# Optimization experiments

Measured on AMD Instinct MI355X. Metric: run time of the kernel, lower is better.

## Reference

```python
import jax, jax.numpy as jnp
import numpy as np

NUM_HEADS = 16


def setup_inputs() -> dict:
    key = jax.random.key(0)
    ks = jax.random.split(key, 5)
    B, S, D = 2, 2048, 2048
    scale = 1.0 / np.sqrt(D)
    return {
        "x": jax.random.normal(ks[0], (B, S, D), dtype=jnp.float32),
        "W_q": jax.random.normal(ks[1], (D, D), dtype=jnp.float32) * scale,
        "W_k": jax.random.normal(ks[2], (D, D), dtype=jnp.float32) * scale,
        "W_v": jax.random.normal(ks[3], (D, D), dtype=jnp.float32) * scale,
        "W_o": jax.random.normal(ks[4], (D, D), dtype=jnp.float32) * scale,
        "b_o": jnp.zeros((D,), dtype=jnp.float32),
    }


def reference(x, W_q, W_k, W_v, W_o, b_o):
    B, S, D = x.shape
    H = NUM_HEADS
    hd = D // H
    # projections, split into heads: [B, H, S, hd]
    q = (x @ W_q).reshape(B, S, H, hd).transpose(0, 2, 1, 3)
    k = (x @ W_k).reshape(B, S, H, hd).transpose(0, 2, 1, 3)
    v = (x @ W_v).reshape(B, S, H, hd).transpose(0, 2, 1, 3)
    # causal attention with explicit score matrix [B, H, S, S]
    scores = jnp.einsum("bhqd,bhkd->bhqk", q, k) / jnp.sqrt(jnp.asarray(hd, x.dtype))
    causal = jnp.tril(jnp.ones((S, S), dtype=bool))  # True = keep
    scores = jnp.where(causal, scores, -jnp.inf)
    weights = jax.nn.softmax(scores, axis=-1)
    ctx = jnp.einsum("bhqk,bhkd->bhqd", weights, v)
    ctx = ctx.transpose(0, 2, 1, 3).reshape(B, S, D)
    return ctx @ W_o + b_o
```

## Files before the change

### kernel.cpp

```cpp
#include <hip/hip_runtime.h>
#include <stdint.h>

#define SQ_S 2048
#define DIM 2048
#define NH 16
#define HD 128
#define NB 2
#define NROWS (NB * SQ_S)
#define NQKV (3 * DIM)
#define NQK (2 * DIM)

typedef __bf16 bf16x8 __attribute__((ext_vector_type(8)));
typedef float f32x4 __attribute__((ext_vector_type(4)));
typedef unsigned short u16;

__device__ __forceinline__ u16 f2bf(float f) {
    unsigned int u = __float_as_uint(f);
    u += 0x7FFF + ((u >> 16) & 1);
    return (u16)(u >> 16);
}

__device__ __forceinline__ void load_lds16(const u16* g, u16* lds) {
    __builtin_amdgcn_global_load_lds(
        (const __attribute__((address_space(1))) unsigned int*)(uintptr_t)g,
        (__attribute__((address_space(3))) unsigned int*)(unsigned int)(uintptr_t)lds,
        16, 0, 0);
}

__global__ __launch_bounds__(256) void cast_x_kernel(const float* __restrict__ in,
                                                     u16* __restrict__ out) {
    int i = (blockIdx.x * 256 + threadIdx.x) * 4;
    float4 v = *(const float4*)(in + i);
    ushort4 o;
    o.x = f2bf(v.x); o.y = f2bf(v.y); o.z = f2bf(v.z); o.w = f2bf(v.w);
    *(ushort4*)(out + i) = o;
}

__global__ __launch_bounds__(256) void transpose_w_kernel(
    const float* __restrict__ w0, const float* __restrict__ w1,
    const float* __restrict__ w2, const float* __restrict__ w3,
    u16* __restrict__ o0, u16* __restrict__ o1,
    u16* __restrict__ o2, u16* __restrict__ o3) {
    __shared__ u16 tile[64][65];
    int z = blockIdx.z;
    const float* in = z == 0 ? w0 : z == 1 ? w1 : z == 2 ? w2 : w3;
    u16* out = z == 0 ? o0 : z == 1 ? o1 : z == 2 ? o2 : o3;
    int r0 = blockIdx.y * 64, c0 = blockIdx.x * 64;
    int t = threadIdx.x;
#pragma unroll
    for (int i = 0; i < 16; ++i) {
        int idx = i * 256 + t;
        int r = idx >> 6, c = idx & 63;
        tile[r][c] = f2bf(in[(size_t)(r0 + r) * DIM + c0 + c]);
    }
    __syncthreads();
#pragma unroll
    for (int i = 0; i < 4; ++i) {
        int idx = i * 256 + t;
        int oc = idx >> 4;
        int r4 = (idx & 15) * 4;
        ushort4 v;
        v.x = tile[r4 + 0][oc]; v.y = tile[r4 + 1][oc];
        v.z = tile[r4 + 2][oc]; v.w = tile[r4 + 3][oc];
        *(ushort4*)(out + (size_t)(c0 + oc) * DIM + r0 + r4) = v;
    }
}

#define NTK (DIM / 64)

__device__ __forceinline__ bf16x8 frag(const u16* half, int row, int lq) {
    return *(const bf16x8*)(half + row * 32 + (((lq + (row >> 1)) & 3) * 8));
}

__device__ __forceinline__ void stage_half(const u16* __restrict__ G, int grow0, int gcol0,
                                           u16* dst, int t) {
#pragma unroll
    for (int i = 0; i < 2; ++i) {
        int e = (i * 512 + t) * 8;
        int r = e >> 5;
        int c = ((t & 3) - (r >> 1)) & 3;
        load_lds16(G + (size_t)(grow0 + r) * DIM + gcol0 + c * 8, dst + e);
    }
}

#define HSZ (256 * 32)

__global__ __launch_bounds__(512) void gemm_qkv(const u16* __restrict__ A,
                                                const u16* __restrict__ Bt,
                                                u16* __restrict__ QKo,
                                                u16* __restrict__ Vt) {
    __shared__ u16 As[2][2][HSZ];
    __shared__ u16 Bs[2][2][HSZ];
    int bid = blockIdx.x;
    int wg = (bid & 7) * 48 + (bid >> 3);
    int bm = wg / 24, bn = wg % 24;
    int gm0 = bm * 256, gn0 = bn * 256;
    int t = threadIdx.x;
    int w = t >> 6, l = t & 63;
    int wm = w >> 2, wn = w & 3;
    int lr = l & 15, lq = l >> 4;
    int ar = wm * 128 + lr;
    int br = wn * 64 + lr;
    f32x4 acc[8][4] = {};
    bf16x8 af[4], bfr[4];

    stage_half(A,  gm0, 0,  As[0][0], t);
    stage_half(Bt, gn0, 0,  Bs[0][0], t);
    stage_half(A,  gm0, 32, As[0][1], t);
    stage_half(Bt, gn0, 32, Bs[0][1], t);
    asm volatile("s_waitcnt vmcnt(4)" ::: "memory");
    __builtin_amdgcn_s_barrier();

#pragma unroll 2
    for (int kt = 0; kt < NTK; ++kt) {
        int buf = kt & 1, nbuf = buf ^ 1;
        int ks = (kt + 1 < NTK) ? kt + 1 : kt;
#pragma unroll
        for (int kk = 0; kk < 2; ++kk) {
            const u16* ah = As[buf][kk];
            const u16* bh = Bs[buf][kk];
#pragma unroll
            for (int nf = 0; nf < 4; ++nf) bfr[nf] = frag(bh, br + nf * 16, lq);
#pragma unroll
            for (int mf = 0; mf < 4; ++mf) af[mf] = frag(ah, ar + mf * 16, lq);
            stage_half(A, gm0, ks * 64 + kk * 32, As[nbuf][kk], t);
            __builtin_amdgcn_s_barrier();
            __builtin_amdgcn_s_setprio(1);
#pragma unroll
            for (int mf = 0; mf < 4; ++mf)
#pragma unroll
                for (int nf = 0; nf < 4; ++nf)
                    acc[mf][nf] = __builtin_amdgcn_mfma_f32_16x16x32_bf16(af[mf], bfr[nf], acc[mf][nf], 0, 0, 0);
            __builtin_amdgcn_s_setprio(0);
            __builtin_amdgcn_s_barrier();
#pragma unroll
            for (int mf = 0; mf < 4; ++mf) af[mf] = frag(ah, ar + 64 + mf * 16, lq);
            stage_half(Bt, gn0, ks * 64 + kk * 32, Bs[nbuf][kk], t);
            asm volatile("s_waitcnt vmcnt(4)" ::: "memory");
            __builtin_amdgcn_s_barrier();
            __builtin_amdgcn_s_setprio(1);
#pragma unroll
            for (int mf = 0; mf < 4; ++mf)
#pragma unroll
                for (int nf = 0; nf < 4; ++nf)
                    acc[mf + 4][nf] = __builtin_amdgcn_mfma_f32_16x16x32_bf16(af[mf], bfr[nf], acc[mf + 4][nf], 0, 0, 0);
            __builtin_amdgcn_s_setprio(0);
            __builtin_amdgcn_s_barrier();
        }
    }
    asm volatile("s_waitcnt vmcnt(0)" ::: "memory");

    int c0g = gn0 + wn * 64;
    int r0g = gm0 + wm * 128;
    if (bn < 16) {
#pragma unroll
        for (int mf = 0; mf < 8; ++mf)
#pragma unroll
            for (int nf = 0; nf < 4; ++nf) {
                int col = c0g + nf * 16 + lr;
                int rowb = r0g + mf * 16 + lq * 4;
#pragma unroll
                for (int r = 0; r < 4; ++r)
                    QKo[(size_t)(rowb + r) * NQK + col] = f2bf(acc[mf][nf][r]);
            }
    } else {
#pragma unroll
        for (int mf = 0; mf < 8; ++mf)
#pragma unroll
            for (int nf = 0; nf < 4; ++nf) {
                int colv = c0g + nf * 16 + lr - 4096;
                int h = colv >> 7, dd = colv & 127;
                int rowb = r0g + mf * 16 + lq * 4;
                int b = rowb >> 11, s = rowb & 2047;
                ushort4 v4;
                v4.x = f2bf(acc[mf][nf][0]);
                v4.y = f2bf(acc[mf][nf][1]);
                v4.z = f2bf(acc[mf][nf][2]);
                v4.w = f2bf(acc[mf][nf][3]);
                *(ushort4*)(Vt + (((size_t)(b * NH + h) * HD + dd) * SQ_S + s)) = v4;
            }
    }
}

#define ASZ (256 * 32)
#define BSZ (128 * 32)

__device__ __forceinline__ void stage_b128(const u16* __restrict__ Bt, int gn0, int kt, int kk,
                                           u16* dst, int t) {
    int e = t * 8;
    int r = e >> 5;
    int c = ((t & 3) - (r >> 1)) & 3;
    load_lds16(Bt + (size_t)(gn0 + r) * DIM + kt * 64 + kk * 32 + c * 8, dst + e);
}

__device__ __forceinline__ void gemm_core(const u16* __restrict__ A, const u16* __restrict__ Bt,
                                          int gm0, int gn0, u16* As, u16* Bs,
                                          f32x4 acc[4][4]) {
    int t = threadIdx.x;
    int w = t >> 6, l = t & 63;
    int wm = w >> 1, wn = w & 1;
    int lr = l & 15, lq = l >> 4;
    int ar = wm * 64 + lr;
    int br = wn * 64 + lr;

    stage_half(A, gm0, 0, As + 0 * ASZ, t);
    stage_b128(Bt, gn0, 0, 0, Bs + 0 * BSZ, t);
    stage_half(A, gm0, 32, As + 1 * ASZ, t);
    stage_b128(Bt, gn0, 0, 1, Bs + 1 * BSZ, t);
    stage_half(A, gm0, 64, As + 2 * ASZ, t);
    stage_b128(Bt, gn0, 1, 0, Bs + 2 * BSZ, t);
    asm volatile("s_waitcnt vmcnt(6)" ::: "memory");
    __builtin_amdgcn_s_barrier();

#pragma unroll 2
    for (int kt = 0; kt < NTK; ++kt) {
        int buf = kt & 1, nbuf = buf ^ 1;
        const u16* a0 = As + (buf * 2 + 0) * ASZ;
        const u16* a1 = As + (buf * 2 + 1) * ASZ;
        const u16* b0 = Bs + (buf * 2 + 0) * BSZ;
        const u16* b1 = Bs + (buf * 2 + 1) * BSZ;
        bf16x8 af[4], bfr[4];

#pragma unroll
        for (int mf = 0; mf < 4; ++mf) af[mf] = frag(a0, ar + mf * 16, lq);
#pragma unroll
        for (int nf = 0; nf < 4; ++nf) bfr[nf] = frag(b0, br + nf * 16, lq);
        {
            int ks = (kt + 1 < NTK) ? kt + 1 : kt;
            stage_half(A, gm0, ks * 64 + 32, As + (nbuf * 2 + 1) * ASZ, t);
            stage_b128(Bt, gn0, ks, 1, Bs + (nbuf * 2 + 1) * BSZ, t);
        }
        asm volatile("s_waitcnt vmcnt(6)" ::: "memory");
        __builtin_amdgcn_s_barrier();
        __builtin_amdgcn_s_setprio(1);
#pragma unroll
        for (int mf = 0; mf < 4; ++mf)
#pragma unroll
            for (int nf = 0; nf < 4; ++nf)
                acc[mf][nf] = __builtin_amdgcn_mfma_f32_16x16x32_bf16(af[mf], bfr[nf], acc[mf][nf], 0, 0, 0);
        __builtin_amdgcn_s_setprio(0);
        __builtin_amdgcn_s_barrier();

#pragma unroll
        for (int mf = 0; mf < 4; ++mf) af[mf] = frag(a1, ar + mf * 16, lq);
#pragma unroll
        for (int nf = 0; nf < 4; ++nf) bfr[nf] = frag(b1, br + nf * 16, lq);
        {
            int ks = (kt + 2 < NTK) ? kt + 2 : kt;
            stage_half(A, gm0, ks * 64, As + (buf * 2 + 0) * ASZ, t);
            stage_b128(Bt, gn0, ks, 0, Bs + (buf * 2 + 0) * BSZ, t);
        }
        asm volatile("s_waitcnt vmcnt(6)" ::: "memory");
        __builtin_amdgcn_s_barrier();
        __builtin_amdgcn_s_setprio(1);
#pragma unroll
        for (int mf = 0; mf < 4; ++mf)
#pragma unroll
            for (int nf = 0; nf < 4; ++nf)
                acc[mf][nf] = __builtin_amdgcn_mfma_f32_16x16x32_bf16(af[mf], bfr[nf], acc[mf][nf], 0, 0, 0);
        __builtin_amdgcn_s_setprio(0);
        __builtin_amdgcn_s_barrier();
    }
    asm volatile("s_waitcnt vmcnt(0)" ::: "memory");
}

__global__ __launch_bounds__(512) void gemm_out(const u16* __restrict__ A,
                                                const u16* __restrict__ Bt,
                                                float* __restrict__ C,
                                                const float* __restrict__ bias) {
    __shared__ u16 As[4 * ASZ];
    __shared__ u16 Bs[4 * BSZ];
    int bid = blockIdx.x;
    int wg = (bid & 7) * 32 + (bid >> 3);
    int bm = wg >> 4, bn = wg & 15;
    f32x4 acc[4][4] = {};
    gemm_core(A, Bt, bm * 256, bn * 128, As, Bs, acc);

    int t = threadIdx.x, w = t >> 6, l = t & 63;
    int wm = w >> 1, wn = w & 1, lr = l & 15, lq = l >> 4;
    int r0 = bm * 256 + wm * 64;
    int c0 = bn * 128 + wn * 64;
#pragma unroll
    for (int mf = 0; mf < 4; ++mf)
#pragma unroll
        for (int nf = 0; nf < 4; ++nf) {
            int col = c0 + nf * 16 + lr;
            float bb = bias[col];
            int rowb = r0 + mf * 16 + lq * 4;
#pragma unroll
            for (int r = 0; r < 4; ++r)
                C[(size_t)(rowb + r) * DIM + col] = acc[mf][nf][r] + bb;
        }
}

__global__ __launch_bounds__(256) void attn_kernel(const u16* __restrict__ Q,
                                                   const u16* __restrict__ K,
                                                   const u16* __restrict__ Vt,
                                                   u16* __restrict__ ctx, int ldqk) {
    __shared__ u16 Kl[2][64 * 128];
    __shared__ u16 Vl[2][128 * 64];
    __shared__ u16 Pl[4][16 * 64];
    int t = threadIdx.x;
    int w = t >> 6, l = t & 63;
    int lr = l & 15, q = l >> 4, lk = q * 8;
    int bid = blockIdx.x;
    int r_  = bid >> 3;
    int px  = r_ & 15;
    int h   = (bid & 7) + ((r_ >> 4) & 1) * 8;
    int b   = r_ >> 5;
    const float scale = 0.08838834764831845f;
    int stK_gcol = (((t & 15) ^ (t >> 4)) * 8);
    int stV_gcol = (((t & 7) ^ ((t >> 3) & 7)) * 8);
    const u16* Kbase = K + (size_t)b * SQ_S * ldqk + h * HD;
    const u16* Vbase = Vt + ((size_t)(b * NH + h)) * HD * SQ_S;

    bf16x8 vones;
#pragma unroll
    for (int i = 0; i < 8; ++i) vones[i] = (__bf16)1.0f;

#pragma unroll 1
    for (int pass = 0; pass < 2; ++pass) {
        int qt = pass == 0 ? px : 31 - px;
        int q0 = qt * 64;
        int njt = qt + 1;

        bf16x8 qf[4];
        {
            const u16* qp = Q + ((size_t)(b * SQ_S + q0 + w * 16 + lr)) * ldqk + h * HD;
#pragma unroll
            for (int kd = 0; kd < 4; ++kd)
                qf[kd] = *(const bf16x8*)(qp + kd * 32 + lk);
        }

        f32x4 o[8] = {};
        f32x4 lsum = {0.f, 0.f, 0.f, 0.f};

        {
            int e = t * 8;
#pragma unroll
            for (int c = 0; c < 4; ++c) {
                int eK = c * 2048 + e;
                load_lds16(Kbase + (size_t)(eK >> 7) * ldqk + stK_gcol, Kl[0] + eK);
            }
#pragma unroll
            for (int c = 0; c < 4; ++c) {
                int eV = c * 2048 + e;
                load_lds16(Vbase + (size_t)(eV >> 6) * SQ_S + stV_gcol, Vl[0] + eV);
            }
        }

#pragma unroll 1
        for (int jt = 0; jt < njt; ++jt) {
            __syncthreads();
            if (jt + 1 < njt) {
                int j1 = (jt + 1) * 64;
                u16* Kd = Kl[(jt + 1) & 1];
                u16* Vd = Vl[(jt + 1) & 1];
                int e = t * 8;
#pragma unroll
                for (int c = 0; c < 4; ++c) {
                    int eK = c * 2048 + e;
                    load_lds16(Kbase + (size_t)(j1 + (eK >> 7)) * ldqk + stK_gcol, Kd + eK);
                }
#pragma unroll
                for (int c = 0; c < 4; ++c) {
                    int eV = c * 2048 + e;
                    load_lds16(Vbase + (size_t)(eV >> 6) * SQ_S + j1 + stV_gcol, Vd + eV);
                }
            }
            const u16* Kc = Kl[jt & 1];
            const u16* Vc = Vl[jt & 1];

            f32x4 s[4] = {};
            __builtin_amdgcn_s_setprio(1);
#pragma unroll
            for (int kd = 0; kd < 4; ++kd) {
#pragma unroll
                for (int nt = 0; nt < 4; ++nt) {
                    bf16x8 kb = *(const bf16x8*)(Kc + (nt * 16 + lr) * 128 +
                                                 (((kd * 4 + q) ^ lr) * 8));
                    s[nt] = __builtin_amdgcn_mfma_f32_16x16x32_bf16(qf[kd], kb, s[nt], 0, 0, 0);
                }
            }
            __builtin_amdgcn_s_setprio(0);
            bool diag = (jt == qt);
            float pv[4][4];
#pragma unroll
            for (int nt = 0; nt < 4; ++nt)
#pragma unroll
                for (int r = 0; r < 4; ++r) {
                    float v = s[nt][r] * scale - 6.0f;
                    if (diag && (nt * 16 + lr > w * 16 + q * 4 + r)) v = -1.0e30f;
                    pv[nt][r] = __expf(v);
                }
            u16* pw = Pl[w];
#pragma unroll
            for (int nt = 0; nt < 4; ++nt)
#pragma unroll
                for (int r = 0; r < 4; ++r) {
                    int prow = q * 4 + r;
                    int pcol = nt * 16 + lr;
                    pw[prow * 64 + (((pcol >> 3) ^ (prow & 7)) * 8) + (pcol & 7)] = f2bf(pv[nt][r]);
                }
            asm volatile("s_waitcnt lgkmcnt(0)" ::: "memory");
            __builtin_amdgcn_s_setprio(1);
#pragma unroll
            for (int kj = 0; kj < 2; ++kj) {
                bf16x8 pa = *(const bf16x8*)(pw + lr * 64 + (((kj * 4 + q) ^ (lr & 7)) * 8));
                lsum = __builtin_amdgcn_mfma_f32_16x16x32_bf16(pa, vones, lsum, 0, 0, 0);
#pragma unroll
                for (int nd = 0; nd < 8; ++nd) {
                    bf16x8 vb = *(const bf16x8*)(Vc + (nd * 16 + lr) * 64 +
                                                 (((kj * 4 + q) ^ (lr & 7)) * 8));
                    o[nd] = __builtin_amdgcn_mfma_f32_16x16x32_bf16(pa, vb, o[nd], 0, 0, 0);
                }
            }
            __builtin_amdgcn_s_setprio(0);
        }
        float li[4];
#pragma unroll
        for (int r = 0; r < 4; ++r) li[r] = 1.f / lsum[r];
#pragma unroll
        for (int nd = 0; nd < 8; ++nd)
#pragma unroll
            for (int r = 0; r < 4; ++r) {
                int row = q0 + w * 16 + q * 4 + r;
                int col = h * HD + nd * 16 + lr;
                ctx[((size_t)(b * SQ_S + row)) * DIM + col] = f2bf(o[nd][r] * li[r]);
            }
        __syncthreads();
    }
}

extern "C" void kernel_launch(void* const* d_in, const int* in_sizes, int n_in,
                              void* d_out, int out_size, void* d_ws, size_t ws_size,
                              hipStream_t stream) {
    const float* x  = (const float*)d_in[0];
    const float* Wq = (const float*)d_in[1];
    const float* Wk = (const float*)d_in[2];
    const float* Wv = (const float*)d_in[3];
    const float* Wo = (const float*)d_in[4];
    const float* bo = (const float*)d_in[5];
    float* out = (float*)d_out;

    char* p = (char*)d_ws;
    const size_t SZ_ACT = (size_t)NROWS * DIM * 2;
    const size_t SZ_W   = (size_t)DIM * DIM * 2;
    u16* Xb   = (u16*)(p);
    u16* Wqkv = (u16*)(p + SZ_ACT);
    u16* Wot  = (u16*)(p + SZ_ACT + 3 * SZ_W);
    u16* QK   = (u16*)(p + SZ_ACT + 4 * SZ_W);
    u16* Vt   = (u16*)(p + 3 * SZ_ACT + 4 * SZ_W);
    u16* Cx   = (u16*)(p + 4 * SZ_ACT + 4 * SZ_W);

    cast_x_kernel<<<(NROWS * DIM) / 1024, 256, 0, stream>>>(x, Xb);
    transpose_w_kernel<<<dim3(DIM / 64, DIM / 64, 4), 256, 0, stream>>>(
        Wq, Wk, Wv, Wo,
        Wqkv, Wqkv + (size_t)DIM * DIM, Wqkv + 2 * (size_t)DIM * DIM, Wot);
    gemm_qkv<<<384, 512, 0, stream>>>(Xb, Wqkv, QK, Vt);
    attn_kernel<<<512, 256, 0, stream>>>(QK, QK + DIM, Vt, Cx, NQK);
    gemm_out<<<256, 512, 0, stream>>>(Cx, Wot, out, bo);
}
```

Baseline: 352.4 us.

## Retile QKV GEMM to 128x384 blocks for even wave coverage

Changes the QKV projection GEMM tile from 256x256 to 128x384 and launches 512 blocks instead of 384. Blocks are remapped so each XCD owns two column tiles, and A and B staging now happen in a single step per k-half instead of two. The epilogue now picks between the Q/K and V-transposed output for each 16-column fragment, since a 384-wide tile can straddle the V boundary. The aim is to fill the 256 CUs in whole waves rather than 1.5, at the cost of fewer FLOPs per staged byte and a shorter overlap window for loads.

Measured after the change: 355.5 us. About the same (+0.9%).

```diff
diff --git a/kernel.cpp b/kernel.cpp
--- a/kernel.cpp
+++ b/kernel.cpp
@@ -83,31 +83,52 @@
     }
 }
 
-#define HSZ (256 * 32)
+__device__ __forceinline__ void stage_a128(const u16* __restrict__ G, int grow0, int gcol0,
+                                           u16* dst, int t) {
+    int e = t * 8;
+    int r = e >> 5;
+    int c = ((t & 3) - (r >> 1)) & 3;
+    load_lds16(G + (size_t)(grow0 + r) * DIM + gcol0 + c * 8, dst + e);
+}
+
+__device__ __forceinline__ void stage_b384(const u16* __restrict__ G, int grow0, int gcol0,
+                                           u16* dst, int t) {
+#pragma unroll
+    for (int i = 0; i < 3; ++i) {
+        int e = (i * 512 + t) * 8;
+        int r = e >> 5;
+        int c = ((t & 3) - (r >> 1)) & 3;
+        load_lds16(G + (size_t)(grow0 + r) * DIM + gcol0 + c * 8, dst + e);
+    }
+}
+
+#define HSA (128 * 32)
+#define HSB (384 * 32)
 
 __global__ __launch_bounds__(512) void gemm_qkv(const u16* __restrict__ A,
                                                 const u16* __restrict__ Bt,
                                                 u16* __restrict__ QKo,
                                                 u16* __restrict__ Vt) {
-    __shared__ u16 As[2][2][HSZ];
-    __shared__ u16 Bs[2][2][HSZ];
+    __shared__ u16 As[2][2][HSA];
+    __shared__ u16 Bs[2][2][HSB];
     int bid = blockIdx.x;
-    int wg = (bid & 7) * 48 + (bid >> 3);
-    int bm = wg / 24, bn = wg % 24;
-    int gm0 = bm * 256, gn0 = bn * 256;
+    int xcd = bid & 7, idx = bid >> 3;
+    int bn = xcd * 2 + (idx >> 5);
+    int bm = idx & 31;
+    int gm0 = bm * 128, gn0 = bn * 384;
     int t = threadIdx.x;
     int w = t >> 6, l = t & 63;
     int wm = w >> 2, wn = w & 3;
     int lr = l & 15, lq = l >> 4;
-    int ar = wm * 128 + lr;
-    int br = wn * 64 + lr;
-    f32x4 acc[8][4] = {};
-    bf16x8 af[4], bfr[4];
-
-    stage_half(A,  gm0, 0,  As[0][0], t);
-    stage_half(Bt, gn0, 0,  Bs[0][0], t);
-    stage_half(A,  gm0, 32, As[0][1], t);
-    stage_half(Bt, gn0, 32, Bs[0][1], t);
+    int ar = wm * 64 + lr;
+    int br = wn * 96 + lr;
+    f32x4 acc[4][6] = {};
+    bf16x8 af[4], bfr[6];
+
+    stage_a128(A,  gm0, 0,  As[0][0], t);
+    stage_b384(Bt, gn0, 0,  Bs[0][0], t);
+    stage_a128(A,  gm0, 32, As[0][1], t);
+    stage_b384(Bt, gn0, 32, Bs[0][1], t);
     asm volatile("s_waitcnt vmcnt(4)" ::: "memory");
     __builtin_amdgcn_s_barrier();
 
@@ -120,57 +141,40 @@
             const u16* ah = As[buf][kk];
             const u16* bh = Bs[buf][kk];
 #pragma unroll
-            for (int nf = 0; nf < 4; ++nf) bfr[nf] = frag(bh, br + nf * 16, lq);
+            for (int nf = 0; nf < 6; ++nf) bfr[nf] = frag(bh, br + nf * 16, lq);
 #pragma unroll
             for (int mf = 0; mf < 4; ++mf) af[mf] = frag(ah, ar + mf * 16, lq);
-            stage_half(A, gm0, ks * 64 + kk * 32, As[nbuf][kk], t);
+            stage_a128(A,  gm0, ks * 64 + kk * 32, As[nbuf][kk], t);
+            stage_b384(Bt, gn0, ks * 64 + kk * 32, Bs[nbuf][kk], t);
+            asm volatile("s_waitcnt vmcnt(4)" ::: "memory");
             __builtin_amdgcn_s_barrier();
             __builtin_amdgcn_s_setprio(1);
 #pragma unroll
             for (int mf = 0; mf < 4; ++mf)
 #pragma unroll
-                for (int nf = 0; nf < 4; ++nf)
+                for (int nf = 0; nf < 6; ++nf)
                     acc[mf][nf] = __builtin_amdgcn_mfma_f32_16x16x32_bf16(af[mf], bfr[nf], acc[mf][nf], 0, 0, 0);
             __builtin_amdgcn_s_setprio(0);
             __builtin_amdgcn_s_barrier();
-#pragma unroll
-            for (int mf = 0; mf < 4; ++mf) af[mf] = frag(ah, ar + 64 + mf * 16, lq);
-            stage_half(Bt, gn0, ks * 64 + kk * 32, Bs[nbuf][kk], t);
-            asm volatile("s_waitcnt vmcnt(4)" ::: "memory");
-            __builtin_amdgcn_s_barrier();
-            __builtin_amdgcn_s_setprio(1);
-#pragma unroll
-            for (int mf = 0; mf < 4; ++mf)
-#pragma unroll
-                for (int nf = 0; nf < 4; ++nf)
-                    acc[mf + 4][nf] = __builtin_amdgcn_mfma_f32_16x16x32_bf16(af[mf], bfr[nf], acc[mf + 4][nf], 0, 0, 0);
-            __builtin_amdgcn_s_setprio(0);
-            __builtin_amdgcn_s_barrier();
         }
     }
     asm volatile("s_waitcnt vmcnt(0)" ::: "memory");
 
-    int c0g = gn0 + wn * 64;
-    int r0g = gm0 + wm * 128;
-    if (bn < 16) {
-#pragma unroll
-        for (int mf = 0; mf < 8; ++mf)
-#pragma unroll
-            for (int nf = 0; nf < 4; ++nf) {
-                int col = c0g + nf * 16 + lr;
-                int rowb = r0g + mf * 16 + lq * 4;
+    int r0g = gm0 + wm * 64;
+#pragma unroll
+    for (int mf = 0; mf < 4; ++mf)
+#pragma unroll
+        for (int nf = 0; nf < 6; ++nf) {
+            int base = gn0 + wn * 96 + nf * 16;
+            int rowb = r0g + mf * 16 + lq * 4;
+            if (base < 4096) {
+                int col = base + lr;
 #pragma unroll
                 for (int r = 0; r < 4; ++r)
                     QKo[(size_t)(rowb + r) * NQK + col] = f2bf(acc[mf][nf][r]);
-            }
-    } else {
-#pragma unroll
-        for (int mf = 0; mf < 8; ++mf)
-#pragma unroll
-            for (int nf = 0; nf < 4; ++nf) {
-                int colv = c0g + nf * 16 + lr - 4096;
+            } else {
+                int colv = base + lr - 4096;
                 int h = colv >> 7, dd = colv & 127;
-                int rowb = r0g + mf * 16 + lq * 4;
                 int b = rowb >> 11, s = rowb & 2047;
                 ushort4 v4;
                 v4.x = f2bf(acc[mf][nf][0]);
@@ -179,7 +183,7 @@
                 v4.w = f2bf(acc[mf][nf][3]);
                 *(ushort4*)(Vt + (((size_t)(b * NH + h) * HD + dd) * SQ_S + s)) = v4;
             }
-    }
+        }
 }
 
 #define ASZ (256 * 32)
@@ -457,7 +461,7 @@
     transpose_w_kernel<<<dim3(DIM / 64, DIM / 64, 4), 256, 0, stream>>>(
         Wq, Wk, Wv, Wo,
         Wqkv, Wqkv + (size_t)DIM * DIM, Wqkv + 2 * (size_t)DIM * DIM, Wot);
-    gemm_qkv<<<384, 512, 0, stream>>>(Xb, Wqkv, QK, Vt);
+    gemm_qkv<<<512, 512, 0, stream>>>(Xb, Wqkv, QK, Vt);
     attn_kernel<<<512, 256, 0, stream>>>(QK, QK + DIM, Vt, Cx, NQK);
     gemm_out<<<256, 512, 0, stream>>>(Cx, Wot, out, bo);
 }
```

## Process 128 query rows per attention block to reuse K/V tiles

Applied to the files above, without the earlier changes.

The attention kernel now gives each block a 128-row query tile, held as two 64-row halves, instead of two paired 64-row passes. Every K/V tile staged in LDS feeds twice as many MFMAs, which halves the global-to-LDS traffic per unit of work. Blocks are ordered with the longest causal tiles first to replace the old pair-balancing scheme. The cost is higher register pressure from doubled accumulators and Q fragments, and coarser load balancing across blocks.

Measured after the change: 378.7 us. 1.07x slower.

```diff
diff --git a/kernel.cpp b/kernel.cpp
--- a/kernel.cpp
+++ b/kernel.cpp
@@ -299,15 +299,16 @@
                                                    u16* __restrict__ ctx, int ldqk) {
     __shared__ u16 Kl[2][64 * 128];
     __shared__ u16 Vl[2][128 * 64];
-    __shared__ u16 Pl[4][16 * 64];
+    __shared__ u16 Pl[4 * 2 * 16 * 64];
     int t = threadIdx.x;
     int w = t >> 6, l = t & 63;
     int lr = l & 15, q = l >> 4, lk = q * 8;
     int bid = blockIdx.x;
-    int r_  = bid >> 3;
-    int px  = r_ & 15;
-    int h   = (bid & 7) + ((r_ >> 4) & 1) * 8;
-    int b   = r_ >> 5;
+    int qt = 15 - (bid >> 5);
+    int bh = bid & 31;
+    int b  = bh >> 4, h = bh & 15;
+    int q0 = qt * 128;
+    int njt = 2 * qt + 2;
     const float scale = 0.08838834764831845f;
     int stK_gcol = (((t & 15) ^ (t >> 4)) * 8);
     int stV_gcol = (((t & 7) ^ ((t >> 3) & 7)) * 8);
@@ -318,118 +319,143 @@
 #pragma unroll
     for (int i = 0; i < 8; ++i) vones[i] = (__bf16)1.0f;
 
+    bf16x8 qf0[4], qf1[4];
+    {
+        const u16* qp0 = Q + ((size_t)(b * SQ_S + q0 + w * 16 + lr)) * ldqk + h * HD;
+        const u16* qp1 = qp0 + (size_t)64 * ldqk;
+#pragma unroll
+        for (int kd = 0; kd < 4; ++kd) {
+            qf0[kd] = *(const bf16x8*)(qp0 + kd * 32 + lk);
+            qf1[kd] = *(const bf16x8*)(qp1 + kd * 32 + lk);
+        }
+    }
+
+    f32x4 o0[8] = {}, o1[8] = {};
+    f32x4 lsum0 = {0.f, 0.f, 0.f, 0.f}, lsum1 = {0.f, 0.f, 0.f, 0.f};
+    u16* pw0 = Pl + (w * 2 + 0) * 1024;
+    u16* pw1 = Pl + (w * 2 + 1) * 1024;
+
+    {
+        int e = t * 8;
+#pragma unroll
+        for (int c = 0; c < 4; ++c) {
+            int eK = c * 2048 + e;
+            load_lds16(Kbase + (size_t)(eK >> 7) * ldqk + stK_gcol, Kl[0] + eK);
+        }
+#pragma unroll
+        for (int c = 0; c < 4; ++c) {
+            int eV = c * 2048 + e;
+            load_lds16(Vbase + (size_t)(eV >> 6) * SQ_S + stV_gcol, Vl[0] + eV);
+        }
+    }
+
 #pragma unroll 1
-    for (int pass = 0; pass < 2; ++pass) {
-        int qt = pass == 0 ? px : 31 - px;
-        int q0 = qt * 64;
-        int njt = qt + 1;
-
-        bf16x8 qf[4];
-        {
-            const u16* qp = Q + ((size_t)(b * SQ_S + q0 + w * 16 + lr)) * ldqk + h * HD;
-#pragma unroll
-            for (int kd = 0; kd < 4; ++kd)
-                qf[kd] = *(const bf16x8*)(qp + kd * 32 + lk);
-        }
-
-        f32x4 o[8] = {};
-        f32x4 lsum = {0.f, 0.f, 0.f, 0.f};
-
-        {
+    for (int jt = 0; jt < njt; ++jt) {
+        __syncthreads();
+        if (jt + 1 < njt) {
+            int j1 = (jt + 1) * 64;
+            u16* Kd = Kl[(jt + 1) & 1];
+            u16* Vd = Vl[(jt + 1) & 1];
             int e = t * 8;
 #pragma unroll
             for (int c = 0; c < 4; ++c) {
                 int eK = c * 2048 + e;
-                load_lds16(Kbase + (size_t)(eK >> 7) * ldqk + stK_gcol, Kl[0] + eK);
+                load_lds16(Kbase + (size_t)(j1 + (eK >> 7)) * ldqk + stK_gcol, Kd + eK);
             }
 #pragma unroll
             for (int c = 0; c < 4; ++c) {
                 int eV = c * 2048 + e;
-                load_lds16(Vbase + (size_t)(eV >> 6) * SQ_S + stV_gcol, Vl[0] + eV);
-            }
-        }
-
-#pragma unroll 1
-        for (int jt = 0; jt < njt; ++jt) {
-            __syncthreads();
-            if (jt + 1 < njt) {
-                int j1 = (jt + 1) * 64;
-                u16* Kd = Kl[(jt + 1) & 1];
-                u16* Vd = Vl[(jt + 1) & 1];
-                int e = t * 8;
-#pragma unroll
-                for (int c = 0; c < 4; ++c) {
-                    int eK = c * 2048 + e;
-                    load_lds16(Kbase + (size_t)(j1 + (eK >> 7)) * ldqk + stK_gcol, Kd + eK);
-                }
-#pragma unroll
-                for (int c = 0; c < 4; ++c) {
-                    int eV = c * 2048 + e;
-                    load_lds16(Vbase + (size_t)(eV >> 6) * SQ_S + j1 + stV_gcol, Vd + eV);
-                }
-            }
-            const u16* Kc = Kl[jt & 1];
-            const u16* Vc = Vl[jt & 1];
-
-            f32x4 s[4] = {};
-            __builtin_amdgcn_s_setprio(1);
-#pragma unroll
-            for (int kd = 0; kd < 4; ++kd) {
-#pragma unroll
-                for (int nt = 0; nt < 4; ++nt) {
-                    bf16x8 kb = *(const bf16x8*)(Kc + (nt * 16 + lr) * 128 +
-                                                 (((kd * 4 + q) ^ lr) * 8));
-                    s[nt] = __builtin_amdgcn_mfma_f32_16x16x32_bf16(qf[kd], kb, s[nt], 0, 0, 0);
-                }
-            }
-            __builtin_amdgcn_s_setprio(0);
-            bool diag = (jt == qt);
+                load_lds16(Vbase + (size_t)(eV >> 6) * SQ_S + j1 + stV_gcol, Vd + eV);
+            }
+        }
+        const u16* Kc = Kl[jt & 1];
+        const u16* Vc = Vl[jt & 1];
+
+        f32x4 s0[4] = {}, s1[4] = {};
+        __builtin_amdgcn_s_setprio(1);
+#pragma unroll
+        for (int kd = 0; kd < 4; ++kd) {
+#pragma unroll
+            for (int nt = 0; nt < 4; ++nt) {
+                bf16x8 kb = *(const bf16x8*)(Kc + (nt * 16 + lr) * 128 +
+                                             (((kd * 4 + q) ^ lr) * 8));
+                s0[nt] = __builtin_amdgcn_mfma_f32_16x16x32_bf16(qf0[kd], kb, s0[nt], 0, 0, 0);
+                s1[nt] = __builtin_amdgcn_mfma_f32_16x16x32_bf16(qf1[kd], kb, s1[nt], 0, 0, 0);
+            }
+        }
+        __builtin_amdgcn_s_setprio(0);
+
+        int jb = jt * 64 - q0;
+        {
+            bool dom0 = (jt >= 2 * qt);
             float pv[4][4];
 #pragma unroll
             for (int nt = 0; nt < 4; ++nt)
 #pragma unroll
                 for (int r = 0; r < 4; ++r) {
-                    float v = s[nt][r] * scale - 6.0f;
-                    if (diag && (nt * 16 + lr > w * 16 + q * 4 + r)) v = -1.0e30f;
+                    float v = s0[nt][r] * scale - 6.0f;
+                    if (dom0 && (jb + nt * 16 + lr > w * 16 + q * 4 + r)) v = -1.0e30f;
                     pv[nt][r] = __expf(v);
                 }
-            u16* pw = Pl[w];
 #pragma unroll
             for (int nt = 0; nt < 4; ++nt)
 #pragma unroll
                 for (int r = 0; r < 4; ++r) {
                     int prow = q * 4 + r;
                     int pcol = nt * 16 + lr;
-                    pw[prow * 64 + (((pcol >> 3) ^ (prow & 7)) * 8) + (pcol & 7)] = f2bf(pv[nt][r]);
+                    pw0[prow * 64 + (((pcol >> 3) ^ (prow & 7)) * 8) + (pcol & 7)] = f2bf(pv[nt][r]);
                 }
-            asm volatile("s_waitcnt lgkmcnt(0)" ::: "memory");
-            __builtin_amdgcn_s_setprio(1);
-#pragma unroll
-            for (int kj = 0; kj < 2; ++kj) {
-                bf16x8 pa = *(const bf16x8*)(pw + lr * 64 + (((kj * 4 + q) ^ (lr & 7)) * 8));
-                lsum = __builtin_amdgcn_mfma_f32_16x16x32_bf16(pa, vones, lsum, 0, 0, 0);
-#pragma unroll
-                for (int nd = 0; nd < 8; ++nd) {
-                    bf16x8 vb = *(const bf16x8*)(Vc + (nd * 16 + lr) * 64 +
-                                                 (((kj * 4 + q) ^ (lr & 7)) * 8));
-                    o[nd] = __builtin_amdgcn_mfma_f32_16x16x32_bf16(pa, vb, o[nd], 0, 0, 0);
+        }
+        {
+            bool dom1 = (jt >= 2 * qt + 1);
+            float pv[4][4];
+#pragma unroll
+            for (int nt = 0; nt < 4; ++nt)
+#pragma unroll
+                for (int r = 0; r < 4; ++r) {
+                    float v = s1[nt][r] * scale - 6.0f;
+                    if (dom1 && (jb + nt * 16 + lr > 64 + w * 16 + q * 4 + r)) v = -1.0e30f;
+                    pv[nt][r] = __expf(v);
                 }
-            }
-            __builtin_amdgcn_s_setprio(0);
-        }
-        float li[4];
-#pragma unroll
-        for (int r = 0; r < 4; ++r) li[r] = 1.f / lsum[r];
-#pragma unroll
-        for (int nd = 0; nd < 8; ++nd)
-#pragma unroll
-            for (int r = 0; r < 4; ++r) {
-                int row = q0 + w * 16 + q * 4 + r;
-                int col = h * HD + nd * 16 + lr;
-                ctx[((size_t)(b * SQ_S + row)) * DIM + col] = f2bf(o[nd][r] * li[r]);
-            }
-        __syncthreads();
-    }
+#pragma unroll
+            for (int nt = 0; nt < 4; ++nt)
+#pragma unroll
+                for (int r = 0; r < 4; ++r) {
+                    int prow = q * 4 + r;
+                    int pcol = nt * 16 + lr;
+                    pw1[prow * 64 + (((pcol >> 3) ^ (prow & 7)) * 8) + (pcol & 7)] = f2bf(pv[nt][r]);
+                }
+        }
+        asm volatile("s_waitcnt lgkmcnt(0)" ::: "memory");
+        __builtin_amdgcn_s_setprio(1);
+#pragma unroll
+        for (int kj = 0; kj < 2; ++kj) {
+            bf16x8 pa0 = *(const bf16x8*)(pw0 + lr * 64 + (((kj * 4 + q) ^ (lr & 7)) * 8));
+            bf16x8 pa1 = *(const bf16x8*)(pw1 + lr * 64 + (((kj * 4 + q) ^ (lr & 7)) * 8));
+            lsum0 = __builtin_amdgcn_mfma_f32_16x16x32_bf16(pa0, vones, lsum0, 0, 0, 0);
+            lsum1 = __builtin_amdgcn_mfma_f32_16x16x32_bf16(pa1, vones, lsum1, 0, 0, 0);
+#pragma unroll
+            for (int nd = 0; nd < 8; ++nd) {
+                bf16x8 vb = *(const bf16x8*)(Vc + (nd * 16 + lr) * 64 +
+                                             (((kj * 4 + q) ^ (lr & 7)) * 8));
+                o0[nd] = __builtin_amdgcn_mfma_f32_16x16x32_bf16(pa0, vb, o0[nd], 0, 0, 0);
+                o1[nd] = __builtin_amdgcn_mfma_f32_16x16x32_bf16(pa1, vb, o1[nd], 0, 0, 0);
+            }
+        }
+        __builtin_amdgcn_s_setprio(0);
+    }
+    float li0[4], li1[4];
+#pragma unroll
+    for (int r = 0; r < 4; ++r) { li0[r] = 1.f / lsum0[r]; li1[r] = 1.f / lsum1[r]; }
+#pragma unroll
+    for (int nd = 0; nd < 8; ++nd)
+#pragma unroll
+        for (int r = 0; r < 4; ++r) {
+            int row0 = q0 + w * 16 + q * 4 + r;
+            int col = h * HD + nd * 16 + lr;
+            ctx[((size_t)(b * SQ_S + row0)) * DIM + col] = f2bf(o0[nd][r] * li0[r]);
+            ctx[((size_t)(b * SQ_S + row0 + 64)) * DIM + col] = f2bf(o1[nd][r] * li1[r]);
+        }
 }
 
 extern "C" void kernel_launch(void* const* d_in, const int* in_sizes, int n_in,
```

## Replace double-buffered QKV GEMM pipeline with single-buffer staging and higher occupancy

Applied to the files above, without the earlier changes.

The QKV projection GEMM drops its double-buffered, barrier-interleaved LDS prefetch. Each k-tile is now staged fully into a single LDS buffer and fenced with __syncthreads before compute. This halves LDS use and adds a launch-bounds hint for 4 blocks per CU, aiming to hide memory latency through occupancy rather than software pipelining. The cost is that load and MFMA no longer overlap within a block. The higher occupancy target may also squeeze registers enough to spill the large 128-float accumulator.

New measurement: 1.389 ms. +294.1%, slower.

```diff
diff --git a/kernel.cpp b/kernel.cpp
--- a/kernel.cpp
+++ b/kernel.cpp
@@ -85,12 +85,12 @@
 
 #define HSZ (256 * 32)
 
-__global__ __launch_bounds__(512) void gemm_qkv(const u16* __restrict__ A,
-                                                const u16* __restrict__ Bt,
-                                                u16* __restrict__ QKo,
-                                                u16* __restrict__ Vt) {
-    __shared__ u16 As[2][2][HSZ];
-    __shared__ u16 Bs[2][2][HSZ];
+__global__ __launch_bounds__(512, 4) void gemm_qkv(const u16* __restrict__ A,
+                                                   const u16* __restrict__ Bt,
+                                                   u16* __restrict__ QKo,
+                                                   u16* __restrict__ Vt) {
+    __shared__ u16 As[2][HSZ];
+    __shared__ u16 Bs[2][HSZ];
     int bid = blockIdx.x;
     int wg = (bid & 7) * 48 + (bid >> 3);
     int bm = wg / 24, bn = wg % 24;
@@ -104,27 +104,19 @@
     f32x4 acc[8][4] = {};
     bf16x8 af[4], bfr[4];
 
-    stage_half(A,  gm0, 0,  As[0][0], t);
-    stage_half(Bt, gn0, 0,  Bs[0][0], t);
-    stage_half(A,  gm0, 32, As[0][1], t);
-    stage_half(Bt, gn0, 32, Bs[0][1], t);
-    asm volatile("s_waitcnt vmcnt(4)" ::: "memory");
-    __builtin_amdgcn_s_barrier();
-
-#pragma unroll 2
+#pragma unroll 1
     for (int kt = 0; kt < NTK; ++kt) {
-        int buf = kt & 1, nbuf = buf ^ 1;
-        int ks = (kt + 1 < NTK) ? kt + 1 : kt;
+        stage_half(A,  gm0, kt * 64,      As[0], t);
+        stage_half(A,  gm0, kt * 64 + 32, As[1], t);
+        stage_half(Bt, gn0, kt * 64,      Bs[0], t);
+        stage_half(Bt, gn0, kt * 64 + 32, Bs[1], t);
+        __syncthreads();
 #pragma unroll
         for (int kk = 0; kk < 2; ++kk) {
-            const u16* ah = As[buf][kk];
-            const u16* bh = Bs[buf][kk];
-#pragma unroll
-            for (int nf = 0; nf < 4; ++nf) bfr[nf] = frag(bh, br + nf * 16, lq);
-#pragma unroll
-            for (int mf = 0; mf < 4; ++mf) af[mf] = frag(ah, ar + mf * 16, lq);
-            stage_half(A, gm0, ks * 64 + kk * 32, As[nbuf][kk], t);
-            __builtin_amdgcn_s_barrier();
+#pragma unroll
+            for (int nf = 0; nf < 4; ++nf) bfr[nf] = frag(Bs[kk], br + nf * 16, lq);
+#pragma unroll
+            for (int mf = 0; mf < 4; ++mf) af[mf] = frag(As[kk], ar + mf * 16, lq);
             __builtin_amdgcn_s_setprio(1);
 #pragma unroll
             for (int mf = 0; mf < 4; ++mf)
@@ -132,12 +124,8 @@
                 for (int nf = 0; nf < 4; ++nf)
                     acc[mf][nf] = __builtin_amdgcn_mfma_f32_16x16x32_bf16(af[mf], bfr[nf], acc[mf][nf], 0, 0, 0);
             __builtin_amdgcn_s_setprio(0);
-            __builtin_amdgcn_s_barrier();
-#pragma unroll
-            for (int mf = 0; mf < 4; ++mf) af[mf] = frag(ah, ar + 64 + mf * 16, lq);
-            stage_half(Bt, gn0, ks * 64 + kk * 32, Bs[nbuf][kk], t);
-            asm volatile("s_waitcnt vmcnt(4)" ::: "memory");
-            __builtin_amdgcn_s_barrier();
+#pragma unroll
+            for (int mf = 0; mf < 4; ++mf) af[mf] = frag(As[kk], ar + 64 + mf * 16, lq);
             __builtin_amdgcn_s_setprio(1);
 #pragma unroll
             for (int mf = 0; mf < 4; ++mf)
@@ -145,10 +133,9 @@
                 for (int nf = 0; nf < 4; ++nf)
                     acc[mf + 4][nf] = __builtin_amdgcn_mfma_f32_16x16x32_bf16(af[mf], bfr[nf], acc[mf + 4][nf], 0, 0, 0);
             __builtin_amdgcn_s_setprio(0);
-            __builtin_amdgcn_s_barrier();
-        }
-    }
-    asm volatile("s_waitcnt vmcnt(0)" ::: "memory");
+        }
+        __syncthreads();
+    }
 
     int c0g = gn0 + wn * 64;
     int r0g = gm0 + wm * 128;
```
